# Optimization experiments

Measured on AMD Instinct MI355X. Metric: run time of the kernel, lower is better.

## Reference

```python
import jax, jax.numpy as jnp
import numpy as np

NB, NX, NU, NY, NQ = 16384, 512, 256, 128, 256


def setup_inputs() -> dict:
    key = jax.random.key(0)
    ks = jax.random.split(key, 13)
    s = 0.02  # small weight scale keeps the tanh recurrence well-behaved
    x = jax.random.normal(ks[0], (NB, NX), jnp.float32)
    u = jax.random.normal(ks[1], (NB, NU), jnp.float32)
    F = jax.random.normal(ks[2], (NX, NX), jnp.float32) * s
    B1 = jax.random.normal(ks[3], (NX, NQ), jnp.float32) * s
    B2 = jax.random.normal(ks[4], (NX, NU), jnp.float32) * s
    C1 = jax.random.normal(ks[5], (NQ, NX), jnp.float32) * s
    C2 = jax.random.normal(ks[6], (NY, NX), jnp.float32) * s
    D11 = jax.random.normal(ks[7], (NQ, NQ), jnp.float32) * s
    D12 = jax.random.normal(ks[8], (NQ, NU), jnp.float32) * s
    D21 = jax.random.normal(ks[9], (NY, NQ), jnp.float32) * s
    # E must be invertible (torch.inverse(self.E)); identity + small perturbation
    E = jnp.eye(NX, dtype=jnp.float32) + 0.05 * jax.random.normal(ks[10], (NX, NX), jnp.float32)
    # Lambda diagonal, positive (only Lambda[k,k] is used in _solve_w)
    lam = jax.random.uniform(ks[11], (NQ,), jnp.float32, minval=0.5, maxval=1.5)
    bv = jnp.zeros((NQ,), jnp.float32)  # bias=False -> bv is zeros
    return dict(x=x, u=u, F=F, B1=B1, B2=B2, C1=C1, C2=C2, D11=D11,
                D12=D12, D21=D21, E=E, lam=lam, bv=bv)


def _solve_w(x, u, C1, D11, D12, lam, bv):
    # Sequential forward-substitution over the nq nonlinear states:
    #   v_k = (x@C1[k] + w@D11[k] + u@D12[k] + bv[k]) / Lambda[k,k];  w_k = tanh(v_k)
    nb = x.shape[0]
    nq = lam.shape[0]
    # x/u contributions do not depend on w: precompute once. [nb, nq]
    xu = x @ C1.T + u @ D12.T + bv[None, :]

    def step(w, inp):
        d11_row, xu_k, lam_k, k = inp
        v_k = (xu_k + w @ d11_row) / lam_k          # [nb]
        w = w.at[:, k].set(jnp.tanh(v_k))
        return w, None

    w0 = jnp.zeros((nb, nq), x.dtype)
    w, _ = jax.lax.scan(step, w0, (D11, xu.T, lam, jnp.arange(nq)))
    return w


def reference(x, u, F, B1, B2, C1, C2, D11, D12, D21, E, lam, bv):
    w = _solve_w(x, u, C1, D11, D12, lam, bv)
    E_inv = jnp.linalg.inv(E)
    dx = x @ (E_inv @ F).T + w @ (E_inv @ B1).T + u @ (E_inv @ B2).T
    # linear_output path (no feedthrough: D22 term omitted as in default D22=0)
    y = x @ C2.T + w @ D21.T
    return dx, y
```

## Files before the change

kernel.cpp:

```cpp
#include <hip/hip_runtime.h>

#define NBq 16384
#define NXq 512
#define NUq 256
#define NYq 128
#define NQq 256
#define KP  1024
#define AUGW 1536

typedef __attribute__((ext_vector_type(8))) short short8;
typedef __attribute__((ext_vector_type(4))) float f32x4;

__device__ __forceinline__ ushort f2bf(float f) {
  uint x = __float_as_uint(f);
  x += 0x7FFFu + ((x >> 16) & 1u);
  return (ushort)(x >> 16);
}

#define GLOAD_LDS16(g, l)                                             \
  __builtin_amdgcn_global_load_lds(                                   \
      (const __attribute__((address_space(1))) void*)(g),             \
      (__attribute__((address_space(3))) void*)(l), 16, 0, 0)

__device__ __forceinline__ float rdlane(float x, int l) {
  return __int_as_float(__builtin_amdgcn_readlane(__float_as_int(x), l));
}

__device__ __forceinline__ void invert64(float (*M)[132], float (*pinv)[17], int tid) {
  const int wave = tid >> 6, lane = tid & 63;
  const int R4 = (tid >> 4) * 4;
  const int C8 = (tid & 15) * 8;
  for (int t = 0; t < 4; ++t) {
    const int kt = t * 16;
    if (wave == 0) {
      const int cc = lane & 31;
      float q[16];
      #pragma unroll
      for (int r = 0; r < 16; ++r)
        q[r] = (cc < 16) ? M[kt + r][kt + cc] : ((r == cc - 16) ? 1.f : 0.f);
      #pragma unroll
      for (int p = 0; p < 16; ++p) {
        float piv = rdlane(q[p], p);
        float rp = __builtin_amdgcn_rcpf(piv);
        rp = rp * (2.f - piv * rp);
        float a[16];
        #pragma unroll
        for (int r = 0; r < 16; ++r) a[r] = rdlane(q[r], p);
        q[p] *= rp;
        #pragma unroll
        for (int r = 0; r < 16; ++r)
          if (r != p) q[r] = fmaf(-a[r], q[p], q[r]);
      }
      if (lane >= 16 && lane < 32) {
        #pragma unroll
        for (int r = 0; r < 16; ++r) pinv[r][lane - 16] = q[r];
      }
    }
    __syncthreads();
    {
      const int ri = tid >> 4, j0 = (tid & 15) * 8;
      float rr[8] = {};
      float a0[8], a1[8], p0, p1;
      p0 = pinv[ri][0];
      #pragma unroll
      for (int c = 0; c < 8; c += 4)
        *(float4*)(&a0[c]) = *(const float4*)(&M[kt][j0 + c]);
      #pragma unroll
      for (int k = 0; k < 16; k += 2) {
        p1 = pinv[ri][k + 1];
        #pragma unroll
        for (int c = 0; c < 8; c += 4)
          *(float4*)(&a1[c]) = *(const float4*)(&M[kt + k + 1][j0 + c]);
        #pragma unroll
        for (int c = 0; c < 8; ++c) rr[c] = fmaf(p0, a0[c], rr[c]);
        if (k + 2 < 16) {
          p0 = pinv[ri][k + 2];
          #pragma unroll
          for (int c = 0; c < 8; c += 4)
            *(float4*)(&a0[c]) = *(const float4*)(&M[kt + k + 2][j0 + c]);
        }
        #pragma unroll
        for (int c = 0; c < 8; ++c) rr[c] = fmaf(p1, a1[c], rr[c]);
      }
      __syncthreads();
      #pragma unroll
      for (int c = 0; c < 8; c += 4)
        *(float4*)(&M[kt + ri][j0 + c]) = make_float4(rr[c], rr[c+1], rr[c+2], rr[c+3]);
    }
    __syncthreads();
    {
      const bool act = (wave != t);
      float mult[4][16], o2[4][8];
      if (act) {
        #pragma unroll
        for (int r = 0; r < 4; ++r) {
          #pragma unroll
          for (int j = 0; j < 4; ++j) {
            float4 m4 = *(const float4*)(&M[R4 + r][kt + 4 * j]);
            mult[r][4*j+0] = m4.x; mult[r][4*j+1] = m4.y;
            mult[r][4*j+2] = m4.z; mult[r][4*j+3] = m4.w;
          }
          float4 a = *(const float4*)(&M[R4 + r][C8]);
          float4 b = *(const float4*)(&M[R4 + r][C8 + 4]);
          o2[r][0] = a.x; o2[r][1] = a.y; o2[r][2] = a.z; o2[r][3] = a.w;
          o2[r][4] = b.x; o2[r][5] = b.y; o2[r][6] = b.z; o2[r][7] = b.w;
        }
      }
      __syncthreads();
      if (act) {
        float rv[2][8];
        {
          float4 a = *(const float4*)(&M[kt][C8]);
          float4 b = *(const float4*)(&M[kt][C8 + 4]);
          rv[0][0] = a.x; rv[0][1] = a.y; rv[0][2] = a.z; rv[0][3] = a.w;
          rv[0][4] = b.x; rv[0][5] = b.y; rv[0][6] = b.z; rv[0][7] = b.w;
        }
        #pragma unroll
        for (int k = 0; k < 16; ++k) {
          if (k + 1 < 16) {
            float4 a = *(const float4*)(&M[kt + k + 1][C8]);
            float4 b = *(const float4*)(&M[kt + k + 1][C8 + 4]);
            rv[(k+1)&1][0] = a.x; rv[(k+1)&1][1] = a.y;
            rv[(k+1)&1][2] = a.z; rv[(k+1)&1][3] = a.w;
            rv[(k+1)&1][4] = b.x; rv[(k+1)&1][5] = b.y;
            rv[(k+1)&1][6] = b.z; rv[(k+1)&1][7] = b.w;
          }
          #pragma unroll
          for (int r = 0; r < 4; ++r)
            #pragma unroll
            for (int c = 0; c < 8; ++c)
              o2[r][c] = fmaf(-mult[r][k], rv[k&1][c], o2[r][c]);
        }
        #pragma unroll
        for (int r = 0; r < 4; ++r) {
          *(float4*)(&M[R4 + r][C8]) =
              make_float4(o2[r][0], o2[r][1], o2[r][2], o2[r][3]);
          *(float4*)(&M[R4 + r][C8 + 4]) =
              make_float4(o2[r][4], o2[r][5], o2[r][6], o2[r][7]);
        }
      }
    }
    __syncthreads();
  }
}

__global__ __launch_bounds__(256) void k_prep(const float* __restrict__ x, const float* __restrict__ u,
                                              const float* __restrict__ E, const float* __restrict__ F,
                                              const float* __restrict__ B1, const float* __restrict__ B2,
                                              const float* __restrict__ C1, const float* __restrict__ C2,
                                              const float* __restrict__ D11, const float* __restrict__ D12,
                                              const float* __restrict__ D21,
                                              ushort* __restrict__ P, float* __restrict__ AUG,
                                              ushort* __restrict__ Wxu, ushort* __restrict__ D11B,
                                              ushort* __restrict__ Wfull, float* __restrict__ DinvG) {
  __shared__ float Mi[64][132];
  __shared__ float pinv[16][17];
  int b = blockIdx.x, tid = threadIdx.x;
  if (b == 17152) {
    const int r = tid >> 2, cq = (tid & 3) * 16;
    #pragma unroll
    for (int c = 0; c < 16; c += 4)
      *(float4*)(&Mi[r][cq + c]) = *(const float4*)(E + (size_t)r * 512 + cq + c);
    #pragma unroll
    for (int c = 0; c < 16; ++c)
      Mi[r][64 + cq + c] = (r == cq + c) ? 1.f : 0.f;
    __syncthreads();
    invert64(Mi, pinv, tid);
    #pragma unroll
    for (int c = 0; c < 16; c += 4)
      *(float4*)(DinvG + (size_t)r * 64 + cq + c) = *(float4*)(&Mi[r][64 + cq + c]);
    return;
  }
  if (b < 12288) {
    int idx = b * 256 + tid;
    const int nx4 = NBq * NXq / 4;
    if (idx < nx4) {
      float4 v = *(const float4*)(x + (size_t)idx * 4);
      int row = idx >> 7, c4 = idx & 127;
      ushort4 h = { f2bf(v.x), f2bf(v.y), f2bf(v.z), f2bf(v.w) };
      *(ushort4*)(P + (size_t)row * KP + c4 * 4) = h;
    } else {
      int i = idx - nx4;
      float4 v = *(const float4*)(u + (size_t)i * 4);
      int row = i >> 6, c4 = i & 63;
      ushort4 h = { f2bf(v.x), f2bf(v.y), f2bf(v.z), f2bf(v.w) };
      *(ushort4*)(P + (size_t)row * KP + 768 + c4 * 4) = h;
    }
  } else if (b < 15360) {
    int idx = (b - 12288) * 256 + tid;
    int r = idx / AUGW, c = idx % AUGW;
    float v;
    if (c < 512)       v = E[r * 512 + c];
    else if (c < 1024) v = F[r * 512 + (c - 512)];
    else if (c < 1280) v = B1[r * 256 + (c - 1024)];
    else               v = B2[r * 256 + (c - 1280)];
    AUG[idx] = v;
  } else if (b < 16384) {
    int idx = (b - 15360) * 256 + tid;
    int r = idx >> 10, k = idx & 1023;
    float v;
    if (k < 512)      v = C1[r * 512 + k];
    else if (k < 768) v = 0.f;
    else              v = D12[r * 256 + (k - 768)];
    Wxu[idx] = f2bf(v);
  } else if (b < 16640) {
    int idx = (b - 16384) * 256 + tid;
    D11B[idx] = f2bf(D11[idx]);
  } else {
    int idx = (b - 16640) * 256 + tid;
    int j = idx >> 10, k = idx & 1023;
    float v;
    if (k < 512)      v = C2[j * 512 + k];
    else if (k < 768) v = D21[j * 256 + (k - 512)];
    else              v = 0.f;
    Wfull[(size_t)(512 + j) * KP + k] = f2bf(v);
  }
}

#define WSTRIDE 264
#define TANH_K 2.8853900817779268f

struct Pre {
  f32x4 xuv;
  short8 b[8];
  f32x4 rl2, bv2;
};

template<int t>
__device__ __forceinline__ void tile_loads(const float* __restrict__ xu,
                                           const ushort* __restrict__ D11B,
                                           const float* __restrict__ lam,
                                           const float* __restrict__ bv,
                                           int lane, int r0w, Pre& pre) {
  constexpr int kt = t * 16;
  constexpr int cmax = (t + 1) >> 1;
  const int mr = lane & 15, kq = lane >> 4, q = lane & 3;
  pre.xuv = *(const f32x4*)(&xu[(size_t)(r0w + mr) * NQq + kt + kq * 4]);
  #pragma unroll
  for (int c = 0; c < cmax; ++c)
    pre.b[c] = *(const short8*)(D11B + (size_t)(kt + mr) * NQq + c * 32 + kq * 8);
  float4 l4 = *(const float4*)(&lam[kt + q * 4]);
  float4 b4 = *(const float4*)(&bv[kt + q * 4]);
  pre.rl2[0] = TANH_K / l4.x; pre.rl2[1] = TANH_K / l4.y;
  pre.rl2[2] = TANH_K / l4.z; pre.rl2[3] = TANH_K / l4.w;
  pre.bv2[0] = b4.x * pre.rl2[0]; pre.bv2[1] = b4.y * pre.rl2[1];
  pre.bv2[2] = b4.z * pre.rl2[2]; pre.bv2[3] = b4.w * pre.rl2[3];
}

#define SOLVE_STEP(k, dvreg)                                                   \
  {                                                                            \
    float wb_ = __int_as_float(__builtin_amdgcn_update_dpp(                    \
        0, __float_as_int(wreg), (((k - 1) >> 2) * 0x55), 0xF, 0xF, true));    \
    acc[0] = fmaf(dvreg.x, wb_, acc[0]);                                       \
    acc[1] = fmaf(dvreg.y, wb_, acc[1]);                                       \
    acc[2] = fmaf(dvreg.z, wb_, acc[2]);                                       \
    acc[3] = fmaf(dvreg.w, wb_, acc[3]);                                       \
    if constexpr ((k) + 3 <= 14) dvreg = *(const float4*)(&dT[(k) + 3][q4]);   \
    float v_ = fmaf(acc[(k) & 3], rl2[(k) & 3], bv2[(k) & 3]);                 \
    float e_ = __builtin_amdgcn_exp2f(v_);                                     \
    float w_ = fmaf(-2.f, __builtin_amdgcn_rcpf(1.f + e_), 1.f);               \
    wreg = w_;                                                                 \
    if (q == ((k) >> 2)) wk[(k) & 3] = w_;                                     \
  }

template<int t>
__device__ __forceinline__ void do_tile(const float* __restrict__ xu,
                                        const ushort* __restrict__ D11B,
                                        const float* __restrict__ lam,
                                        const float* __restrict__ bv,
                                        ushort* wb, const float (*d11T)[16][16],
                                        short8 (&whiF)[8], int lane, int bp4,
                                        int r0w, Pre& cur, Pre& nxt) {
  constexpr int kt = t * 16;
  constexpr int cmax = (t + 1) >> 1;
  if constexpr (t < 15)
    tile_loads<t + 1>(xu, D11B, lam, bv, lane, r0w, nxt);
  const int q = lane & 3, r2 = lane >> 2;
  const int q4 = q * 4;
  const float (*dT)[16] = d11T[t];
  float4 dvb0 = *(const float4*)(&dT[0][q4]);
  float4 dvb1 = *(const float4*)(&dT[1][q4]);
  float4 dvb2 = *(const float4*)(&dT[2][q4]);
  float4 dvb3 = *(const float4*)(&dT[3][q4]);
  f32x4 accM = cur.xuv;
  #pragma unroll
  for (int c = 0; c < cmax; ++c)
    accM = __builtin_amdgcn_mfma_f32_16x16x32_bf16(cur.b[c], whiF[c], accM, 0, 0, 0);
  f32x4 acc;
  acc[0] = __int_as_float(__builtin_amdgcn_ds_bpermute(bp4, __float_as_int(accM[0])));
  acc[1] = __int_as_float(__builtin_amdgcn_ds_bpermute(bp4, __float_as_int(accM[1])));
  acc[2] = __int_as_float(__builtin_amdgcn_ds_bpermute(bp4, __float_as_int(accM[2])));
  acc[3] = __int_as_float(__builtin_amdgcn_ds_bpermute(bp4, __float_as_int(accM[3])));
  const f32x4 rl2 = cur.rl2, bv2 = cur.bv2;
  float wreg = 0.f, wk[4] = {0.f, 0.f, 0.f, 0.f};
  {
    float v_ = fmaf(acc[0], rl2[0], bv2[0]);
    float e_ = __builtin_amdgcn_exp2f(v_);
    float w_ = fmaf(-2.f, __builtin_amdgcn_rcpf(1.f + e_), 1.f);
    wreg = w_;
    if (q == 0) wk[0] = w_;
  }
  SOLVE_STEP(1, dvb0)
  SOLVE_STEP(2, dvb1)
  SOLVE_STEP(3, dvb2)
  SOLVE_STEP(4, dvb3)
  SOLVE_STEP(5, dvb0)
  SOLVE_STEP(6, dvb1)
  SOLVE_STEP(7, dvb2)
  SOLVE_STEP(8, dvb3)
  SOLVE_STEP(9, dvb0)
  SOLVE_STEP(10, dvb1)
  SOLVE_STEP(11, dvb2)
  SOLVE_STEP(12, dvb3)
  SOLVE_STEP(13, dvb0)
  SOLVE_STEP(14, dvb1)
  SOLVE_STEP(15, dvb2)
  ushort4 h = { f2bf(wk[0]), f2bf(wk[1]), f2bf(wk[2]), f2bf(wk[3]) };
  *(ushort4*)(wb + r2 * WSTRIDE + kt + q * 4) = h;
  if (((lane >> 4) >> 1) == (t & 1)) {
    constexpr int c = t >> 1;
    whiF[c] = *(const short8*)(wb + (lane & 15) * WSTRIDE + c * 32 + (lane >> 4) * 8);
  }
}

__global__ __launch_bounds__(256) void k_fused(const float* __restrict__ Ain, float* __restrict__ Aout,
                                               ushort* __restrict__ Wfull, int s, int ebase,
                                               ushort* __restrict__ P, const ushort* __restrict__ Wxu,
                                               float* __restrict__ xu,
                                               const float* __restrict__ D11,
                                               const ushort* __restrict__ D11B,
                                               const float* __restrict__ lam,
                                               const float* __restrict__ bv,
                                               float* __restrict__ DinvG) {
  __shared__ __align__(16) char smem[52288];
  const int tid = threadIdx.x;
  const int wave = tid >> 6, lane = tid & 63;
  const int nby = 23 - s;
  const int last = (s == 7);

  if ((int)blockIdx.y < nby) {
    float (*M)[132] = (float (*)[132])smem;
    float (*sP)[68] = (float (*)[68])(smem + 33792);
    float (*pinv)[17] = (float (*)[17])(smem + 33792 + 17408);
    const int s64 = s * 64, r0 = blockIdx.x * 64, c0 = (s + 1 + blockIdx.y) * 64;
    const int r2 = tid >> 2, cq = (tid & 3) * 16;
    const int R4 = (tid >> 4) * 4;
    const int C4 = (tid & 15) * 4;

    float av4[4][4];
    #pragma unroll
    for (int r = 0; r < 4; ++r) {
      float4 v = *(const float4*)(Ain + (size_t)(r0 + R4 + r) * AUGW + c0 + C4);
      av4[r][0] = v.x; av4[r][1] = v.y; av4[r][2] = v.z; av4[r][3] = v.w;
    }
    #pragma unroll
    for (int c4 = 0; c4 < 4; ++c4) {
      *(float4*)(&sP[r2][cq + c4 * 4]) =
          *(const float4*)(Ain + (size_t)(s64 + r2) * AUGW + c0 + cq + c4 * 4);
      *(float4*)(&M[r2][cq + c4 * 4]) =
          *(const float4*)(Ain + (size_t)(r0 + r2) * AUGW + s64 + cq + c4 * 4);
      *(float4*)(&M[r2][64 + cq + c4 * 4]) =
          *(const float4*)(DinvG + (size_t)s * 4096 + (size_t)r2 * 64 + cq + c4 * 4);
    }
    __syncthreads();

    #define LOADCH_PB(dv, sv, ch)                                             \
      do {                                                                    \
        const int q0_ = (ch) * 4;                                             \
        _Pragma("unroll")                                                     \
        for (int r_ = 0; r_ < 4; ++r_) {                                      \
          float4 d_ = *(const float4*)(&M[R4 + r_][64 + q0_]);                \
          dv[r_][0] = d_.x; dv[r_][1] = d_.y; dv[r_][2] = d_.z; dv[r_][3] = d_.w; \
        }                                                                     \
        _Pragma("unroll")                                                     \
        for (int j_ = 0; j_ < 4; ++j_) {                                      \
          float4 s_ = *(const float4*)(&sP[q0_ + j_][C4]);                    \
          sv[j_][0] = s_.x; sv[j_][1] = s_.y; sv[j_][2] = s_.z; sv[j_][3] = s_.w; \
        }                                                                     \
      } while (0)
    #define LOADCH_MC(dv, sv, ch)                                             \
      do {                                                                    \
        const int q0_ = (ch) * 4;                                             \
        _Pragma("unroll")                                                     \
        for (int r_ = 0; r_ < 4; ++r_) {                                      \
          float4 d_ = *(const float4*)(&M[R4 + r_][q0_]);                     \
          dv[r_][0] = d_.x; dv[r_][1] = d_.y; dv[r_][2] = d_.z; dv[r_][3] = d_.w; \
        }                                                                     \
        _Pragma("unroll")                                                     \
        for (int j_ = 0; j_ < 4; ++j_) {                                      \
          float4 s_ = *(const float4*)(&sP[q0_ + j_][C4]);                    \
          sv[j_][0] = s_.x; sv[j_][1] = s_.y; sv[j_][2] = s_.z; sv[j_][3] = s_.w; \
        }                                                                     \
      } while (0)
    #define FMACH(acc, dv, sv, sgn)                                           \
      do {                                                                    \
        _Pragma("unroll")                                                     \
        for (int j_ = 0; j_ < 4; ++j_)                                        \
          _Pragma("unroll")                                                   \
          for (int r_ = 0; r_ < 4; ++r_)                                      \
            _Pragma("unroll")                                                 \
            for (int c_ = 0; c_ < 4; ++c_)                                    \
              acc[r_][c_] = fmaf(sgn dv[r_][j_], sv[j_][c_], acc[r_][c_]);    \
      } while (0)

    float pb[4][4] = {{0.f}};
    {
      float dvA[4][4], svA[4][4], dvB[4][4], svB[4][4];
      LOADCH_PB(dvA, svA, 0);
      #pragma unroll
      for (int ch = 0; ch < 16; ch += 2) {
        LOADCH_PB(dvB, svB, ch + 1);
        FMACH(pb, dvA, svA, +);
        if (ch + 2 < 16) LOADCH_PB(dvA, svA, ch + 2);
        FMACH(pb, dvB, svB, +);
      }
    }
    __syncthreads();
    #pragma unroll
    for (int r = 0; r < 4; ++r)
      *(float4*)(&sP[R4 + r][C4]) = make_float4(pb[r][0], pb[r][1], pb[r][2], pb[r][3]);
    __syncthreads();

    float o[4][4];
    if (blockIdx.x == (unsigned)s) {
      #pragma unroll
      for (int r = 0; r < 4; ++r)
        #pragma unroll
        for (int c = 0; c < 4; ++c) o[r][c] = pb[r][c];
    } else {
      #pragma unroll
      for (int r = 0; r < 4; ++r)
        #pragma unroll
        for (int c = 0; c < 4; ++c) o[r][c] = av4[r][c];
      float dvA[4][4], svA[4][4], dvB[4][4], svB[4][4];
      LOADCH_MC(dvA, svA, 0);
      #pragma unroll
      for (int ch = 0; ch < 16; ch += 2) {
        LOADCH_MC(dvB, svB, ch + 1);
        FMACH(o, dvA, svA, -);
        if (ch + 2 < 16) LOADCH_MC(dvA, svA, ch + 2);
        FMACH(o, dvB, svB, -);
      }
    }
    #undef LOADCH_PB
    #undef LOADCH_MC
    #undef FMACH
    if (last) {
      int k0 = c0 - 512 + C4;
      #pragma unroll
      for (int r = 0; r < 4; ++r) {
        ushort4 h = { f2bf(o[r][0]), f2bf(o[r][1]), f2bf(o[r][2]), f2bf(o[r][3]) };
        *(ushort4*)(Wfull + (size_t)(r0 + R4 + r) * KP + k0) = h;
      }
    } else {
      #pragma unroll
      for (int r = 0; r < 4; ++r)
        *(float4*)(Aout + (size_t)(r0 + R4 + r) * AUGW + c0 + C4) =
            make_float4(o[r][0], o[r][1], o[r][2], o[r][3]);
    }

    if (s < 7 && blockIdx.x == (unsigned)(s + 1) && blockIdx.y == 0) {
      __syncthreads();
      #pragma unroll
      for (int r = 0; r < 4; ++r)
        *(float4*)(&M[R4 + r][C4]) = make_float4(o[r][0], o[r][1], o[r][2], o[r][3]);
      #pragma unroll
      for (int c = 0; c < 16; ++c)
        M[r2][64 + cq + c] = (r2 == cq + c) ? 1.f : 0.f;
      __syncthreads();
      invert64(M, pinv, tid);
      #pragma unroll
      for (int c = 0; c < 16; c += 4)
        *(float4*)(DinvG + (size_t)(s + 1) * 4096 + (size_t)r2 * 64 + cq + c) =
            *(float4*)(&M[r2][64 + cq + c]);
    }
    return;
  }

  const int g = ebase + ((int)blockIdx.y - nby) * 8 + (int)blockIdx.x;

  if (g < 256) {
    ushort* sA = (ushort*)smem;
    ushort* sB = (ushort*)(smem + 24576);
    const int mb = g >> 1, nb = g & 1;
    int wm = wave & 1, wn = wave >> 1;
    int m0 = mb * 128, n0 = nb * 128;
    int r16 = lane & 15, kq = lane >> 4;
    int lrow = lane >> 2, lseg = lane & 3;
    const ushort* gA0 = P + (size_t)(m0 + wave * 32 + lrow) * KP + lseg * 8;
    const ushort* gA1 = gA0 + 16 * KP;
    const ushort* gB0 = Wxu + (size_t)(n0 + wave * 32 + lrow) * KP + lseg * 8;
    const ushort* gB1 = gB0 + 16 * KP;

    #define STAGE_KB(bi, kb_)                                              \
      do {                                                                 \
        GLOAD_LDS16(gA0 + (kb_) * 32, sA + (bi) * 4096 + wave * 1024);     \
        GLOAD_LDS16(gA1 + (kb_) * 32, sA + (bi) * 4096 + wave * 1024 + 512); \
        GLOAD_LDS16(gB0 + (kb_) * 32, sB + (bi) * 4096 + wave * 1024);     \
        GLOAD_LDS16(gB1 + (kb_) * 32, sB + (bi) * 4096 + wave * 1024 + 512); \
      } while (0)

    f32x4 acc[4][4] = {};
    const int NKB = KP / 32;
    STAGE_KB(0, 0);
    STAGE_KB(1, 1);
    #pragma unroll
    for (int kb = 0; kb < NKB; ++kb) {
      const int bi = kb % 3;
      if (kb + 2 < NKB) {
        STAGE_KB((kb + 2) % 3, kb + 2);
        asm volatile("s_waitcnt vmcnt(8)" ::: "memory");
      } else if (kb + 2 == NKB) {
        asm volatile("s_waitcnt vmcnt(4)" ::: "memory");
      } else {
        asm volatile("s_waitcnt vmcnt(0)" ::: "memory");
      }
      __builtin_amdgcn_s_barrier();
      __builtin_amdgcn_sched_barrier(0);
      short8 af[4], bf[4];
      #pragma unroll
      for (int t = 0; t < 4; ++t) {
        af[t] = *(const short8*)(sA + bi * 4096 + (wm * 64 + t * 16 + r16) * 32 + kq * 8);
        bf[t] = *(const short8*)(sB + bi * 4096 + (wn * 64 + t * 16 + r16) * 32 + kq * 8);
      }
      #pragma unroll
      for (int mt = 0; mt < 4; ++mt)
        #pragma unroll
        for (int nt = 0; nt < 4; ++nt)
          acc[mt][nt] = __builtin_amdgcn_mfma_f32_16x16x32_bf16(af[mt], bf[nt], acc[mt][nt], 0, 0, 0);
      __builtin_amdgcn_sched_barrier(0);
      __builtin_amdgcn_s_barrier();
    }
    #undef STAGE_KB

    #pragma unroll
    for (int mt = 0; mt < 4; ++mt)
      #pragma unroll
      for (int nt = 0; nt < 4; ++nt)
        #pragma unroll
        for (int i = 0; i < 4; ++i) {
          int m = m0 + wm * 64 + mt * 16 + kq * 4 + i;
          int n = n0 + wn * 64 + nt * 16 + r16;
          xu[(size_t)m * NQq + n] = acc[mt][nt][i];
        }
    return;
  }

  if (g >= 336 && g < 592) {
    const int sid = g - 336;
    ushort* wB = (ushort*)smem;
    float (*d11T)[16][16] = (float (*)[16][16])(smem + 33792);
    const int r0w = sid * 64 + wave * 16;
    const int bp4 = (((lane >> 2) | ((lane & 3) << 4)) << 2);
    for (int i = tid; i < 4096; i += 256) {
      int tt = i >> 8, j = (i >> 4) & 15, c = i & 15;
      d11T[tt][j][c] = (c > j) ? D11[(size_t)(tt * 16 + c) * NQq + tt * 16 + j] : 0.f;
    }
    Pre pre0, pre1;
    tile_loads<0>(xu, D11B, lam, bv, lane, r0w, pre0);
    __syncthreads();
    ushort* wb = wB + wave * 16 * WSTRIDE;
    short8 whiF[8] = {};
    do_tile<0>(xu, D11B, lam, bv, wb, d11T, whiF, lane, bp4, r0w, pre0, pre1);
    do_tile<1>(xu, D11B, lam, bv, wb, d11T, whiF, lane, bp4, r0w, pre1, pre0);
    do_tile<2>(xu, D11B, lam, bv, wb, d11T, whiF, lane, bp4, r0w, pre0, pre1);
    do_tile<3>(xu, D11B, lam, bv, wb, d11T, whiF, lane, bp4, r0w, pre1, pre0);
    do_tile<4>(xu, D11B, lam, bv, wb, d11T, whiF, lane, bp4, r0w, pre0, pre1);
    do_tile<5>(xu, D11B, lam, bv, wb, d11T, whiF, lane, bp4, r0w, pre1, pre0);
    do_tile<6>(xu, D11B, lam, bv, wb, d11T, whiF, lane, bp4, r0w, pre0, pre1);
    do_tile<7>(xu, D11B, lam, bv, wb, d11T, whiF, lane, bp4, r0w, pre1, pre0);
    do_tile<8>(xu, D11B, lam, bv, wb, d11T, whiF, lane, bp4, r0w, pre0, pre1);
    do_tile<9>(xu, D11B, lam, bv, wb, d11T, whiF, lane, bp4, r0w, pre1, pre0);
    do_tile<10>(xu, D11B, lam, bv, wb, d11T, whiF, lane, bp4, r0w, pre0, pre1);
    do_tile<11>(xu, D11B, lam, bv, wb, d11T, whiF, lane, bp4, r0w, pre1, pre0);
    do_tile<12>(xu, D11B, lam, bv, wb, d11T, whiF, lane, bp4, r0w, pre0, pre1);
    do_tile<13>(xu, D11B, lam, bv, wb, d11T, whiF, lane, bp4, r0w, pre1, pre0);
    do_tile<14>(xu, D11B, lam, bv, wb, d11T, whiF, lane, bp4, r0w, pre0, pre1);
    do_tile<15>(xu, D11B, lam, bv, wb, d11T, whiF, lane, bp4, r0w, pre1, pre0);
    #pragma unroll
    for (int it = 0; it < 8; ++it) {
      int f = it * 64 + lane;
      int m = f >> 5, k8 = f & 31;
      uint4 v = *(const uint4*)(wb + m * WSTRIDE + k8 * 8);
      *(uint4*)(P + (size_t)(r0w + m) * KP + NXq + k8 * 8) = v;
    }
    return;
  }
}

__global__ __launch_bounds__(256) void k_gemm(const ushort* __restrict__ P, const ushort* __restrict__ W,
                                              float* __restrict__ out) {
  __shared__ ushort sA[3][128 * 32];
  __shared__ ushort sB[3][128 * 32];
  int tid = threadIdx.x;
  int lane = tid & 63, wave = tid >> 6;
  int wm = wave & 1, wn = wave >> 1;
  int m0 = blockIdx.x * 128;
  int n0 = blockIdx.y * 128;
  int r16 = lane & 15, kq = lane >> 4;
  int lrow = lane >> 2, lseg = lane & 3;
  const ushort* gA0 = P + (size_t)(m0 + wave * 32 + lrow) * KP + lseg * 8;
  const ushort* gA1 = gA0 + 16 * KP;
  const ushort* gB0 = W + (size_t)(n0 + wave * 32 + lrow) * KP + lseg * 8;
  const ushort* gB1 = gB0 + 16 * KP;

  #define STAGE_KB(bi, kb_)                                        \
    do {                                                           \
      GLOAD_LDS16(gA0 + (kb_) * 32, &sA[bi][wave * 1024]);         \
      GLOAD_LDS16(gA1 + (kb_) * 32, &sA[bi][wave * 1024 + 512]);   \
      GLOAD_LDS16(gB0 + (kb_) * 32, &sB[bi][wave * 1024]);         \
      GLOAD_LDS16(gB1 + (kb_) * 32, &sB[bi][wave * 1024 + 512]);   \
    } while (0)

  f32x4 acc[4][4] = {};
  const int NKB = KP / 32;
  STAGE_KB(0, 0);
  STAGE_KB(1, 1);
  #pragma unroll
  for (int kb = 0; kb < NKB; ++kb) {
    const int bi = kb % 3;
    if (kb + 2 < NKB) {
      STAGE_KB((kb + 2) % 3, kb + 2);
      asm volatile("s_waitcnt vmcnt(8)" ::: "memory");
    } else if (kb + 2 == NKB) {
      asm volatile("s_waitcnt vmcnt(4)" ::: "memory");
    } else {
      asm volatile("s_waitcnt vmcnt(0)" ::: "memory");
    }
    __builtin_amdgcn_s_barrier();
    __builtin_amdgcn_sched_barrier(0);
    short8 af[4], bf[4];
    #pragma unroll
    for (int t = 0; t < 4; ++t) {
      af[t] = *(const short8*)(&sA[bi][(wm * 64 + t * 16 + r16) * 32 + kq * 8]);
      bf[t] = *(const short8*)(&sB[bi][(wn * 64 + t * 16 + r16) * 32 + kq * 8]);
    }
    #pragma unroll
    for (int mt = 0; mt < 4; ++mt)
      #pragma unroll
      for (int nt = 0; nt < 4; ++nt)
        acc[mt][nt] = __builtin_amdgcn_mfma_f32_16x16x32_bf16(af[mt], bf[nt], acc[mt][nt], 0, 0, 0);
    __builtin_amdgcn_sched_barrier(0);
    __builtin_amdgcn_s_barrier();
  }
  #undef STAGE_KB

  #pragma unroll
  for (int mt = 0; mt < 4; ++mt)
    #pragma unroll
    for (int nt = 0; nt < 4; ++nt)
      #pragma unroll
      for (int i = 0; i < 4; ++i) {
        int m = m0 + wm * 64 + mt * 16 + kq * 4 + i;
        int n = n0 + wn * 64 + nt * 16 + r16;
        float val = acc[mt][nt][i];
        if (n < NXq) out[(size_t)m * NXq + n] = val;
        else out[(size_t)NBq * NXq + (size_t)m * NYq + (n - NXq)] = val;
      }
}

extern "C" void kernel_launch(void* const* d_in, const int* in_sizes, int n_in,
                              void* d_out, int out_size, void* d_ws, size_t ws_size,
                              hipStream_t stream) {
  const float* x   = (const float*)d_in[0];
  const float* u   = (const float*)d_in[1];
  const float* F   = (const float*)d_in[2];
  const float* B1  = (const float*)d_in[3];
  const float* B2  = (const float*)d_in[4];
  const float* C1  = (const float*)d_in[5];
  const float* C2  = (const float*)d_in[6];
  const float* D11 = (const float*)d_in[7];
  const float* D12 = (const float*)d_in[8];
  const float* D21 = (const float*)d_in[9];
  const float* E   = (const float*)d_in[10];
  const float* lam = (const float*)d_in[11];
  const float* bv  = (const float*)d_in[12];

  char* ws = (char*)d_ws;
  ushort* P    = (ushort*)ws;
  float* xu    = (float*)(ws + (size_t)(32u << 20));
  float* AUG0  = (float*)(ws + (size_t)(48u << 20));
  float* AUG1  = (float*)(ws + (size_t)(52u << 20));
  ushort* Wfull = (ushort*)(ws + (size_t)(56u << 20));
  ushort* Wxu   = (ushort*)(ws + (size_t)(58u << 20));
  ushort* D11B  = (ushort*)(ws + (size_t)(59u << 20));
  float* DinvG  = (float*)(ws + (size_t)(60u << 20));
  float* out   = (float*)d_out;
  float* AUGbuf[2] = { AUG0, AUG1 };

  static const int ebase_tab[8] = {0, 72, 152, 240, 336, 440, 552, 672};

  k_prep<<<17153, 256, 0, stream>>>(x, u, E, F, B1, B2, C1, C2, D11, D12, D21,
                                    P, AUG0, Wxu, D11B, Wfull, DinvG);
  for (int s = 0; s < 8; ++s)
    k_fused<<<dim3(8, 32), 256, 0, stream>>>(AUGbuf[s & 1], AUGbuf[(s + 1) & 1],
                                             Wfull, s, ebase_tab[s],
                                             P, Wxu, xu, D11, D11B, lam, bv, DinvG);
  k_gemm<<<dim3(128, 5), 256, 0, stream>>>(P, Wfull, out);
}
```

Before: 342.4 us.

## Split block-elimination tiles into half-width columns and add dedicated pivot-inverse block

The block Gauss-Jordan elimination kernel now processes 64x32 column half-tiles instead of 64x64, doubling the grid to give more blocks per step. The next pivot block's inverse moves from a trailing branch of an update block to a dedicated block (by==63, bx==7) that recomputes its own update redundantly. The E inverse in the prep kernel moves to block 0 so it is scheduled first. The extra-work scheduling table (ebase) and the offsets of the overlapped w-solve tiles are retuned for the larger grid. The aim is better CU occupancy and taking the pivot inverse off the critical path, at the cost of more blocks and reloaded pivot data.

```diff
diff --git a/kernel.cpp b/kernel.cpp
--- a/kernel.cpp
+++ b/kernel.cpp
@@ -156,7 +156,7 @@
   __shared__ float Mi[64][132];
   __shared__ float pinv[16][17];
   int b = blockIdx.x, tid = threadIdx.x;
-  if (b == 17152) {
+  if (b == 0) {
     const int r = tid >> 2, cq = (tid & 3) * 16;
     #pragma unroll
     for (int c = 0; c < 16; c += 4)
@@ -171,8 +171,9 @@
       *(float4*)(DinvG + (size_t)r * 64 + cq + c) = *(float4*)(&Mi[r][64 + cq + c]);
     return;
   }
-  if (b < 12288) {
-    int idx = b * 256 + tid;
+  int bb = b - 1;
+  if (bb < 12288) {
+    int idx = bb * 256 + tid;
     const int nx4 = NBq * NXq / 4;
     if (idx < nx4) {
       float4 v = *(const float4*)(x + (size_t)idx * 4);
@@ -186,8 +187,8 @@
       ushort4 h = { f2bf(v.x), f2bf(v.y), f2bf(v.z), f2bf(v.w) };
       *(ushort4*)(P + (size_t)row * KP + 768 + c4 * 4) = h;
     }
-  } else if (b < 15360) {
-    int idx = (b - 12288) * 256 + tid;
+  } else if (bb < 15360) {
+    int idx = (bb - 12288) * 256 + tid;
     int r = idx / AUGW, c = idx % AUGW;
     float v;
     if (c < 512)       v = E[r * 512 + c];
@@ -195,19 +196,19 @@
     else if (c < 1280) v = B1[r * 256 + (c - 1024)];
     else               v = B2[r * 256 + (c - 1280)];
     AUG[idx] = v;
-  } else if (b < 16384) {
-    int idx = (b - 15360) * 256 + tid;
+  } else if (bb < 16384) {
+    int idx = (bb - 15360) * 256 + tid;
     int r = idx >> 10, k = idx & 1023;
     float v;
     if (k < 512)      v = C1[r * 512 + k];
     else if (k < 768) v = 0.f;
     else              v = D12[r * 256 + (k - 768)];
     Wxu[idx] = f2bf(v);
-  } else if (b < 16640) {
-    int idx = (b - 16384) * 256 + tid;
+  } else if (bb < 16640) {
+    int idx = (bb - 16384) * 256 + tid;
     D11B[idx] = f2bf(D11[idx]);
   } else {
-    int idx = (b - 16640) * 256 + tid;
+    int idx = (bb - 16640) * 256 + tid;
     int j = idx >> 10, k = idx & 1023;
     float v;
     if (k < 512)      v = C2[j * 512 + k];
@@ -335,41 +336,157 @@
   __shared__ __align__(16) char smem[52288];
   const int tid = threadIdx.x;
   const int wave = tid >> 6, lane = tid & 63;
-  const int nby = 23 - s;
-  const int last = (s == 7);
-
-  if ((int)blockIdx.y < nby) {
+  const int nhp = 46 - 2 * s;
+  const int bx = blockIdx.x, by = blockIdx.y;
+
+  #define FMACHN(NR, acc, dv, sv, sgn)                                        \
+    do {                                                                      \
+      _Pragma("unroll")                                                       \
+      for (int j_ = 0; j_ < 4; ++j_)                                          \
+        _Pragma("unroll")                                                     \
+        for (int r_ = 0; r_ < NR; ++r_)                                       \
+          _Pragma("unroll")                                                   \
+          for (int c_ = 0; c_ < 4; ++c_)                                      \
+            acc[r_][c_] = fmaf(sgn dv[r_][j_], sv[j_][c_], acc[r_][c_]);      \
+    } while (0)
+
+  if (s < 7 && by == 63 && bx == 7) {
     float (*M)[132] = (float (*)[132])smem;
     float (*sP)[68] = (float (*)[68])(smem + 33792);
     float (*pinv)[17] = (float (*)[17])(smem + 33792 + 17408);
-    const int s64 = s * 64, r0 = blockIdx.x * 64, c0 = (s + 1 + blockIdx.y) * 64;
+    const int s64 = s * 64, rp = (s + 1) * 64, cp = (s + 1) * 64;
     const int r2 = tid >> 2, cq = (tid & 3) * 16;
     const int R4 = (tid >> 4) * 4;
     const int C4 = (tid & 15) * 4;
-
     float av4[4][4];
     #pragma unroll
     for (int r = 0; r < 4; ++r) {
-      float4 v = *(const float4*)(Ain + (size_t)(r0 + R4 + r) * AUGW + c0 + C4);
+      float4 v = *(const float4*)(Ain + (size_t)(rp + R4 + r) * AUGW + cp + C4);
       av4[r][0] = v.x; av4[r][1] = v.y; av4[r][2] = v.z; av4[r][3] = v.w;
     }
     #pragma unroll
     for (int c4 = 0; c4 < 4; ++c4) {
       *(float4*)(&sP[r2][cq + c4 * 4]) =
-          *(const float4*)(Ain + (size_t)(s64 + r2) * AUGW + c0 + cq + c4 * 4);
+          *(const float4*)(Ain + (size_t)(s64 + r2) * AUGW + cp + cq + c4 * 4);
+      *(float4*)(&M[r2][cq + c4 * 4]) =
+          *(const float4*)(Ain + (size_t)(rp + r2) * AUGW + s64 + cq + c4 * 4);
+      *(float4*)(&M[r2][64 + cq + c4 * 4]) =
+          *(const float4*)(DinvG + (size_t)s * 4096 + (size_t)r2 * 64 + cq + c4 * 4);
+    }
+    __syncthreads();
+    float pb[4][4] = {{0.f}};
+    {
+      float dvA[4][4], svA[4][4], dvB[4][4], svB[4][4];
+      #define LD_P(dv, sv, ch)                                                \
+        do {                                                                  \
+          const int q0_ = (ch) * 4;                                           \
+          _Pragma("unroll")                                                   \
+          for (int r_ = 0; r_ < 4; ++r_) {                                    \
+            float4 d_ = *(const float4*)(&M[R4 + r_][64 + q0_]);              \
+            dv[r_][0] = d_.x; dv[r_][1] = d_.y; dv[r_][2] = d_.z; dv[r_][3] = d_.w; \
+          }                                                                   \
+          _Pragma("unroll")                                                   \
+          for (int j_ = 0; j_ < 4; ++j_) {                                    \
+            float4 s_ = *(const float4*)(&sP[q0_ + j_][C4]);                  \
+            sv[j_][0] = s_.x; sv[j_][1] = s_.y; sv[j_][2] = s_.z; sv[j_][3] = s_.w; \
+          }                                                                   \
+        } while (0)
+      LD_P(dvA, svA, 0);
+      #pragma unroll
+      for (int ch = 0; ch < 16; ch += 2) {
+        LD_P(dvB, svB, ch + 1);
+        FMACHN(4, pb, dvA, svA, +);
+        if (ch + 2 < 16) LD_P(dvA, svA, ch + 2);
+        FMACHN(4, pb, dvB, svB, +);
+      }
+      #undef LD_P
+    }
+    __syncthreads();
+    #pragma unroll
+    for (int r = 0; r < 4; ++r)
+      *(float4*)(&sP[R4 + r][C4]) = make_float4(pb[r][0], pb[r][1], pb[r][2], pb[r][3]);
+    __syncthreads();
+    float o[4][4];
+    #pragma unroll
+    for (int r = 0; r < 4; ++r)
+      #pragma unroll
+      for (int c = 0; c < 4; ++c) o[r][c] = av4[r][c];
+    {
+      float dvA[4][4], svA[4][4], dvB[4][4], svB[4][4];
+      #define LD_M(dv, sv, ch)                                                \
+        do {                                                                  \
+          const int q0_ = (ch) * 4;                                           \
+          _Pragma("unroll")                                                   \
+          for (int r_ = 0; r_ < 4; ++r_) {                                    \
+            float4 d_ = *(const float4*)(&M[R4 + r_][q0_]);                   \
+            dv[r_][0] = d_.x; dv[r_][1] = d_.y; dv[r_][2] = d_.z; dv[r_][3] = d_.w; \
+          }                                                                   \
+          _Pragma("unroll")                                                   \
+          for (int j_ = 0; j_ < 4; ++j_) {                                    \
+            float4 s_ = *(const float4*)(&sP[q0_ + j_][C4]);                  \
+            sv[j_][0] = s_.x; sv[j_][1] = s_.y; sv[j_][2] = s_.z; sv[j_][3] = s_.w; \
+          }                                                                   \
+        } while (0)
+      LD_M(dvA, svA, 0);
+      #pragma unroll
+      for (int ch = 0; ch < 16; ch += 2) {
+        LD_M(dvB, svB, ch + 1);
+        FMACHN(4, o, dvA, svA, -);
+        if (ch + 2 < 16) LD_M(dvA, svA, ch + 2);
+        FMACHN(4, o, dvB, svB, -);
+      }
+      #undef LD_M
+    }
+    __syncthreads();
+    #pragma unroll
+    for (int r = 0; r < 4; ++r)
+      *(float4*)(&M[R4 + r][C4]) = make_float4(o[r][0], o[r][1], o[r][2], o[r][3]);
+    #pragma unroll
+    for (int c = 0; c < 16; ++c)
+      M[r2][64 + cq + c] = (r2 == cq + c) ? 1.f : 0.f;
+    __syncthreads();
+    invert64(M, pinv, tid);
+    #pragma unroll
+    for (int c = 0; c < 16; c += 4)
+      *(float4*)(DinvG + (size_t)(s + 1) * 4096 + (size_t)r2 * 64 + cq + c) =
+          *(float4*)(&M[r2][64 + cq + c]);
+    return;
+  }
+
+  if (by < nhp) {
+    float (*M)[132] = (float (*)[132])smem;
+    float (*sP)[68] = (float (*)[68])(smem + 33792);
+    const int s64 = s * 64, r0 = bx * 64;
+    const int cc0 = (s + 1 + (by >> 1)) * 64 + (by & 1) * 32;
+    const int r2 = tid >> 2, cq = (tid & 3) * 16;
+    const int rs = tid >> 2, cs = (tid & 3) * 8;
+    const int R2 = (tid >> 3) * 2, C4 = (tid & 7) * 4;
+
+    float av2[2][4];
+    #pragma unroll
+    for (int r = 0; r < 2; ++r) {
+      float4 v = *(const float4*)(Ain + (size_t)(r0 + R2 + r) * AUGW + cc0 + C4);
+      av2[r][0] = v.x; av2[r][1] = v.y; av2[r][2] = v.z; av2[r][3] = v.w;
+    }
+    #pragma unroll
+    for (int c4 = 0; c4 < 4; ++c4) {
       *(float4*)(&M[r2][cq + c4 * 4]) =
           *(const float4*)(Ain + (size_t)(r0 + r2) * AUGW + s64 + cq + c4 * 4);
       *(float4*)(&M[r2][64 + cq + c4 * 4]) =
           *(const float4*)(DinvG + (size_t)s * 4096 + (size_t)r2 * 64 + cq + c4 * 4);
     }
-    __syncthreads();
-
-    #define LOADCH_PB(dv, sv, ch)                                             \
+    #pragma unroll
+    for (int c = 0; c < 8; c += 4)
+      *(float4*)(&sP[rs][cs + c]) =
+          *(const float4*)(Ain + (size_t)(s64 + rs) * AUGW + cc0 + cs + c);
+    __syncthreads();
+
+    #define LD_P2(dv, sv, ch)                                                 \
       do {                                                                    \
         const int q0_ = (ch) * 4;                                             \
         _Pragma("unroll")                                                     \
-        for (int r_ = 0; r_ < 4; ++r_) {                                      \
-          float4 d_ = *(const float4*)(&M[R4 + r_][64 + q0_]);                \
+        for (int r_ = 0; r_ < 2; ++r_) {                                      \
+          float4 d_ = *(const float4*)(&M[R2 + r_][64 + q0_]);                \
           dv[r_][0] = d_.x; dv[r_][1] = d_.y; dv[r_][2] = d_.z; dv[r_][3] = d_.w; \
         }                                                                     \
         _Pragma("unroll")                                                     \
@@ -378,12 +495,12 @@
           sv[j_][0] = s_.x; sv[j_][1] = s_.y; sv[j_][2] = s_.z; sv[j_][3] = s_.w; \
         }                                                                     \
       } while (0)
-    #define LOADCH_MC(dv, sv, ch)                                             \
+    #define LD_M2(dv, sv, ch)                                                 \
       do {                                                                    \
         const int q0_ = (ch) * 4;                                             \
         _Pragma("unroll")                                                     \
-        for (int r_ = 0; r_ < 4; ++r_) {                                      \
-          float4 d_ = *(const float4*)(&M[R4 + r_][q0_]);                     \
+        for (int r_ = 0; r_ < 2; ++r_) {                                      \
+          float4 d_ = *(const float4*)(&M[R2 + r_][q0_]);                     \
           dv[r_][0] = d_.x; dv[r_][1] = d_.y; dv[r_][2] = d_.z; dv[r_][3] = d_.w; \
         }                                                                     \
         _Pragma("unroll")                                                     \
@@ -392,92 +509,65 @@
           sv[j_][0] = s_.x; sv[j_][1] = s_.y; sv[j_][2] = s_.z; sv[j_][3] = s_.w; \
         }                                                                     \
       } while (0)
-    #define FMACH(acc, dv, sv, sgn)                                           \
-      do {                                                                    \
-        _Pragma("unroll")                                                     \
-        for (int j_ = 0; j_ < 4; ++j_)                                        \
-          _Pragma("unroll")                                                   \
-          for (int r_ = 0; r_ < 4; ++r_)                                      \
-            _Pragma("unroll")                                                 \
-            for (int c_ = 0; c_ < 4; ++c_)                                    \
-              acc[r_][c_] = fmaf(sgn dv[r_][j_], sv[j_][c_], acc[r_][c_]);    \
-      } while (0)
-
-    float pb[4][4] = {{0.f}};
+
+    float pb[2][4] = {{0.f}};
     {
-      float dvA[4][4], svA[4][4], dvB[4][4], svB[4][4];
-      LOADCH_PB(dvA, svA, 0);
+      float dvA[2][4], svA[4][4], dvB[2][4], svB[4][4];
+      LD_P2(dvA, svA, 0);
       #pragma unroll
       for (int ch = 0; ch < 16; ch += 2) {
-        LOADCH_PB(dvB, svB, ch + 1);
-        FMACH(pb, dvA, svA, +);
-        if (ch + 2 < 16) LOADCH_PB(dvA, svA, ch + 2);
-        FMACH(pb, dvB, svB, +);
-      }
-    }
-    __syncthreads();
-    #pragma unroll
-    for (int r = 0; r < 4; ++r)
-      *(float4*)(&sP[R4 + r][C4]) = make_float4(pb[r][0], pb[r][1], pb[r][2], pb[r][3]);
-    __syncthreads();
-
-    float o[4][4];
-    if (blockIdx.x == (unsigned)s) {
-      #pragma unroll
-      for (int r = 0; r < 4; ++r)
+        LD_P2(dvB, svB, ch + 1);
+        FMACHN(2, pb, dvA, svA, +);
+        if (ch + 2 < 16) LD_P2(dvA, svA, ch + 2);
+        FMACHN(2, pb, dvB, svB, +);
+      }
+    }
+    __syncthreads();
+    #pragma unroll
+    for (int r = 0; r < 2; ++r)
+      *(float4*)(&sP[R2 + r][C4]) = make_float4(pb[r][0], pb[r][1], pb[r][2], pb[r][3]);
+    __syncthreads();
+
+    float o[2][4];
+    if (bx == s) {
+      #pragma unroll
+      for (int r = 0; r < 2; ++r)
         #pragma unroll
         for (int c = 0; c < 4; ++c) o[r][c] = pb[r][c];
     } else {
       #pragma unroll
-      for (int r = 0; r < 4; ++r)
-        #pragma unroll
-        for (int c = 0; c < 4; ++c) o[r][c] = av4[r][c];
-      float dvA[4][4], svA[4][4], dvB[4][4], svB[4][4];
-      LOADCH_MC(dvA, svA, 0);
+      for (int r = 0; r < 2; ++r)
+        #pragma unroll
+        for (int c = 0; c < 4; ++c) o[r][c] = av2[r][c];
+      float dvA[2][4], svA[4][4], dvB[2][4], svB[4][4];
+      LD_M2(dvA, svA, 0);
       #pragma unroll
       for (int ch = 0; ch < 16; ch += 2) {
-        LOADCH_MC(dvB, svB, ch + 1);
-        FMACH(o, dvA, svA, -);
-        if (ch + 2 < 16) LOADCH_MC(dvA, svA, ch + 2);
-        FMACH(o, dvB, svB, -);
-      }
-    }
-    #undef LOADCH_PB
-    #undef LOADCH_MC
-    #undef FMACH
-    if (last) {
-      int k0 = c0 - 512 + C4;
-      #pragma unroll
-      for (int r = 0; r < 4; ++r) {
+        LD_M2(dvB, svB, ch + 1);
+        FMACHN(2, o, dvA, svA, -);
+        if (ch + 2 < 16) LD_M2(dvA, svA, ch + 2);
+        FMACHN(2, o, dvB, svB, -);
+      }
+    }
+    #undef LD_P2
+    #undef LD_M2
+    if (s == 7) {
+      int k0 = cc0 - 512 + C4;
+      #pragma unroll
+      for (int r = 0; r < 2; ++r) {
         ushort4 h = { f2bf(o[r][0]), f2bf(o[r][1]), f2bf(o[r][2]), f2bf(o[r][3]) };
-        *(ushort4*)(Wfull + (size_t)(r0 + R4 + r) * KP + k0) = h;
+        *(ushort4*)(Wfull + (size_t)(r0 + R2 + r) * KP + k0) = h;
       }
     } else {
       #pragma unroll
-      for (int r = 0; r < 4; ++r)
-        *(float4*)(Aout + (size_t)(r0 + R4 + r) * AUGW + c0 + C4) =
+      for (int r = 0; r < 2; ++r)
+        *(float4*)(Aout + (size_t)(r0 + R2 + r) * AUGW + cc0 + C4) =
             make_float4(o[r][0], o[r][1], o[r][2], o[r][3]);
     }
-
-    if (s < 7 && blockIdx.x == (unsigned)(s + 1) && blockIdx.y == 0) {
-      __syncthreads();
-      #pragma unroll
-      for (int r = 0; r < 4; ++r)
-        *(float4*)(&M[R4 + r][C4]) = make_float4(o[r][0], o[r][1], o[r][2], o[r][3]);
-      #pragma unroll
-      for (int c = 0; c < 16; ++c)
-        M[r2][64 + cq + c] = (r2 == cq + c) ? 1.f : 0.f;
-      __syncthreads();
-      invert64(M, pinv, tid);
-      #pragma unroll
-      for (int c = 0; c < 16; c += 4)
-        *(float4*)(DinvG + (size_t)(s + 1) * 4096 + (size_t)r2 * 64 + cq + c) =
-            *(float4*)(&M[r2][64 + cq + c]);
-    }
     return;
   }
 
-  const int g = ebase + ((int)blockIdx.y - nby) * 8 + (int)blockIdx.x;
+  const int g = ebase + (by - nhp) * 8 + bx;
 
   if (g < 256) {
     ushort* sA = (ushort*)smem;
@@ -546,8 +636,8 @@
     return;
   }
 
-  if (g >= 336 && g < 592) {
-    const int sid = g - 336;
+  if (g >= 302 && g < 558) {
+    const int sid = g - 302;
     ushort* wB = (ushort*)smem;
     float (*d11T)[16][16] = (float (*)[16][16])(smem + 33792);
     const int r0w = sid * 64 + wave * 16;
@@ -586,6 +676,7 @@
     }
     return;
   }
+  #undef FMACHN
 }
 
 __global__ __launch_bounds__(256) void k_gemm(const ushort* __restrict__ P, const ushort* __restrict__ W,
@@ -688,12 +779,12 @@
   float* out   = (float*)d_out;
   float* AUGbuf[2] = { AUG0, AUG1 };
 
-  static const int ebase_tab[8] = {0, 72, 152, 240, 336, 440, 552, 672};
+  static const int ebase_tab[8] = {0, 143, 302, 477, 668, 875, 1098, 1337};
 
   k_prep<<<17153, 256, 0, stream>>>(x, u, E, F, B1, B2, C1, C2, D11, D12, D21,
                                     P, AUG0, Wxu, D11B, Wfull, DinvG);
   for (int s = 0; s < 8; ++s)
-    k_fused<<<dim3(8, 32), 256, 0, stream>>>(AUGbuf[s & 1], AUGbuf[(s + 1) & 1],
+    k_fused<<<dim3(8, 64), 256, 0, stream>>>(AUGbuf[s & 1], AUGbuf[(s + 1) & 1],
                                              Wfull, s, ebase_tab[s],
                                              P, Wxu, xu, D11, D11B, lam, bv, DinvG);
   k_gemm<<<dim3(128, 5), 256, 0, stream>>>(P, Wfull, out);
```

Result: slower. 351.4 us (+2.6%).
